# Optimization experiments

Hardware: AMD Instinct MI355X
Metric: run time of the kernel (lower is better)

The kernel has to match this reference:

```python
import jax, jax.numpy as jnp
import numpy as np

B, S, D, H = 2, 2048, 1024, 16
DK = D // H


def setup_inputs() -> dict:
    key = jax.random.key(0)
    ks = jax.random.split(key, 14)
    inp = {
        'query': jax.random.normal(ks[0], (B, S, D), jnp.float32),
        'key': jax.random.normal(ks[1], (B, S, D), jnp.float32),
        'value': jax.random.normal(ks[2], (B, S, D), jnp.float32),
        'mask': jax.random.randint(ks[3], (B, 1, S, S), 0, 2).astype(bool),
        'rel_pos_bias': jax.random.normal(ks[4], (1, H, S, S), jnp.float32),
    }
    scale = 1.0 / np.sqrt(D)
    names = ['Wq', 'bq', 'Wk', 'bk', 'Wv', 'bv', 'Wo', 'bo']
    for i, n in enumerate(names):
        k = ks[5 + i]
        if n.startswith('W'):
            inp[n] = jax.random.normal(k, (D, D), jnp.float32) * scale
        else:
            inp[n] = jnp.zeros((D,), jnp.float32)
    return inp


def reference(query, key, value, mask, rel_pos_bias, Wq, bq, Wk, bk, Wv, bv, Wo, bo):
    # torch Linear: y = x @ W^T + b; W stored [out, in]
    def proj(x, W, b):
        y = x @ W.T + b                       # [B,S,D]
        return y.reshape(B, S, H, DK).transpose(0, 2, 1, 3)  # [B,H,S,DK]

    q = proj(query, Wq, bq)
    k = proj(key, Wk, bk)
    v = proj(value, Wv, bv)

    scores = jnp.einsum('bhqd,bhkd->bhqk', q, k) / jnp.sqrt(jnp.float32(DK))
    scores = scores + rel_pos_bias
    scores = jnp.where(mask, jnp.float32(-1e9), scores)
    p_attn = jax.nn.softmax(scores, axis=-1)
    x = jnp.einsum('bhqk,bhkd->bhqd', p_attn, v)  # [B,H,S,DK]
    x = x.transpose(0, 2, 1, 3).reshape(B, S, D)
    return x @ Wo.T + bo
```

## Files before the change

### kernel.cpp

```cpp
#include <hip/hip_runtime.h>
#include <stdint.h>


typedef _Float16 f16;
typedef _Float16 f16x8 __attribute__((ext_vector_type(8)));
typedef _Float16 f16x4 __attribute__((ext_vector_type(4)));
typedef float f32x4 __attribute__((ext_vector_type(4)));

#define LOG2E 1.44269504088896340736f

__device__ __forceinline__ void gload16(const void* g, void* l) {
  __builtin_amdgcn_global_load_lds(
      (const __attribute__((address_space(1))) unsigned int*)g,
      (__attribute__((address_space(3))) unsigned int*)l, 16, 0, 0);
}

struct CvtSrcs { const float* s[7]; };

__global__ __launch_bounds__(256) void cvt_all(CvtSrcs a, f16* __restrict__ out) {
  const int i = blockIdx.x * 256 + threadIdx.x;
  int r, base;
  if (i < 3145728) { r = i >> 20; base = r << 20; }
  else { r = 3 + ((i - 3145728) >> 18); base = 3145728 + ((r - 3) << 18); }
  const float4 v = ((const float4*)a.s[r])[i - base];
  f16x4 o = {(f16)v.x, (f16)v.y, (f16)v.z, (f16)v.w};
  ((f16x4*)out)[i] = o;
}

__global__ void mask_detect(const uint8_t* __restrict__ m, int* __restrict__ flag) {
  __shared__ int s_off, s_weird;
  const int t = threadIdx.x;
  if (t == 0) { s_off = 0; s_weird = 0; }
  __syncthreads();
  int f_off = 0, f_weird = 0;
  for (int i = t; i < 8192; i += 256) {
    const uint8_t v = m[i];
    if ((i & 3) && v) f_off = 1;
    if (v > 1) f_weird = 1;
  }
  if (f_off) atomicOr(&s_off, 1);
  if (f_weird) atomicOr(&s_weird, 1);
  __syncthreads();
  if (t == 0) *flag = (s_off && !s_weird) ? 1 : 0;
}

__global__ __launch_bounds__(256) void mask_canon(const uint8_t* __restrict__ m,
                                                  uint8_t* __restrict__ out,
                                                  const int* __restrict__ flag) {
  const int i = (blockIdx.x * 256 + threadIdx.x) * 4;
  uchar4 o;
  if (*flag) {
    const uchar4 v = *(const uchar4*)(m + i);
    o = make_uchar4(v.x != 0, v.y != 0, v.z != 0, v.w != 0);
  } else {
    const int4 v = *(const int4*)((const int*)m + i);
    o = make_uchar4(v.x != 0, v.y != 0, v.z != 0, v.w != 0);
  }
  *(uchar4*)(out + i) = o;
}

__global__ __launch_bounds__(256, 2) void gemm_qkv(
    const f16* __restrict__ qh, const f16* __restrict__ kh, const f16* __restrict__ vh,
    const f16* __restrict__ wq, const f16* __restrict__ wk, const f16* __restrict__ wv,
    const float* __restrict__ bq, const float* __restrict__ bk, const float* __restrict__ bv,
    f16* __restrict__ Qp, f16* __restrict__ Kp, f16* __restrict__ Vt) {
  constexpr int K = 1024;
  const int t = threadIdx.x;
  const int w = t >> 6, lane = t & 63, l15 = lane & 15, l4 = lane >> 4;
  const int nt = (int)blockIdx.x % 48;
  const int bm = ((int)blockIdx.x / 48) * 128;
  const int which = nt >> 4;
  const int bn = (nt & 15) * 64;
  const f16* A = which == 0 ? qh : which == 1 ? kh : vh;
  const f16* Bw = which == 0 ? wq : which == 1 ? wk : wv;
  const float* bias = which == 0 ? bq : which == 1 ? bk : bv;

  __shared__ f16 As[2][128 * 32];
  __shared__ f16 Bs[2][64 * 32];

  const f16* a0 = A + (size_t)(bm + (t >> 2)) * K + (t & 3) * 8;
  const f16* a1 = a0 + (size_t)64 * K;
  const f16* b0 = Bw + (size_t)(bn + (t >> 2)) * K + (t & 3) * 8;

  f32x4 acc[2][4];
#pragma unroll
  for (int m = 0; m < 2; ++m)
#pragma unroll
    for (int n = 0; n < 4; ++n) acc[m][n] = (f32x4){0.f, 0.f, 0.f, 0.f};

#define STAGE_G(buf, k0)                          \
  do {                                            \
    gload16(a0 + (k0), &As[buf][w * 512]);        \
    gload16(a1 + (k0), &As[buf][2048 + w * 512]); \
    gload16(b0 + (k0), &Bs[buf][w * 512]);        \
  } while (0)

  STAGE_G(0, 0);
  __syncthreads();
  int cur = 0;
#pragma unroll 1
  for (int kt = 0; kt < 32; ++kt) {
    if (kt < 31) STAGE_G(cur ^ 1, (kt + 1) * 32);
    const f16* ap = &As[cur][(w * 32 + l15) * 32 + l4 * 8];
    const f16* bp = &Bs[cur][l15 * 32 + l4 * 8];
    f16x8 af[2], bfr[4];
#pragma unroll
    for (int m = 0; m < 2; ++m) af[m] = *(const f16x8*)(ap + m * 512);
#pragma unroll
    for (int n = 0; n < 4; ++n) bfr[n] = *(const f16x8*)(bp + n * 512);
#pragma unroll
    for (int m = 0; m < 2; ++m)
#pragma unroll
      for (int n = 0; n < 4; ++n)
        acc[m][n] = __builtin_amdgcn_mfma_f32_16x16x32_f16(af[m], bfr[n], acc[m][n], 0, 0, 0);
    __syncthreads();
    cur ^= 1;
  }
#undef STAGE_G

  const float scale = which == 0 ? 0.125f * LOG2E : 1.0f;
  f16* outp = which == 0 ? Qp : which == 1 ? Kp : Vt;
#pragma unroll
  for (int m = 0; m < 2; ++m) {
    const int r0 = bm + w * 32 + m * 16 + (l4 << 2);
#pragma unroll
    for (int n = 0; n < 4; ++n) {
      const int c = bn + n * 16 + l15;
      const float bv = bias[c];
#pragma unroll
      for (int j = 0; j < 4; ++j) {
        const int r = r0 + j;
        const float v = (acc[m][n][j] + bv) * scale;
        const int b_ = r >> 11, s = r & 2047, h_ = c >> 6, dk = c & 63;
        if (which < 2)
          outp[(((size_t)b_ * 16 + h_) * 2048 + s) * 64 + dk] = (f16)v;
        else
          outp[(((size_t)b_ * 16 + h_) * 64 + dk) * 2048 + s] = (f16)v;
      }
    }
  }
}

__global__ __launch_bounds__(256, 2) void gemm_out(const f16* __restrict__ A,
                                                   const f16* __restrict__ Bw,
                                                   const float* __restrict__ bias,
                                                   float* __restrict__ outp) {
  constexpr int K = 1024;
  const int t = threadIdx.x;
  const int w = t >> 6, lane = t & 63, l15 = lane & 15, l4 = lane >> 4;
  const int bm = (int)(blockIdx.x >> 4) * 128;
  const int bn = (int)(blockIdx.x & 15) * 64;

  __shared__ f16 As[2][128 * 32];
  __shared__ f16 Bs[2][64 * 32];

  const f16* a0 = A + (size_t)(bm + (t >> 2)) * K + (t & 3) * 8;
  const f16* a1 = a0 + (size_t)64 * K;
  const f16* b0 = Bw + (size_t)(bn + (t >> 2)) * K + (t & 3) * 8;

  f32x4 acc[2][4];
#pragma unroll
  for (int m = 0; m < 2; ++m)
#pragma unroll
    for (int n = 0; n < 4; ++n) acc[m][n] = (f32x4){0.f, 0.f, 0.f, 0.f};

#define STAGE_G(buf, k0)                          \
  do {                                            \
    gload16(a0 + (k0), &As[buf][w * 512]);        \
    gload16(a1 + (k0), &As[buf][2048 + w * 512]); \
    gload16(b0 + (k0), &Bs[buf][w * 512]);        \
  } while (0)

  STAGE_G(0, 0);
  __syncthreads();
  int cur = 0;
#pragma unroll 1
  for (int kt = 0; kt < 32; ++kt) {
    if (kt < 31) STAGE_G(cur ^ 1, (kt + 1) * 32);
    const f16* ap = &As[cur][(w * 32 + l15) * 32 + l4 * 8];
    const f16* bp = &Bs[cur][l15 * 32 + l4 * 8];
    f16x8 af[2], bfr[4];
#pragma unroll
    for (int m = 0; m < 2; ++m) af[m] = *(const f16x8*)(ap + m * 512);
#pragma unroll
    for (int n = 0; n < 4; ++n) bfr[n] = *(const f16x8*)(bp + n * 512);
#pragma unroll
    for (int m = 0; m < 2; ++m)
#pragma unroll
      for (int n = 0; n < 4; ++n)
        acc[m][n] = __builtin_amdgcn_mfma_f32_16x16x32_f16(af[m], bfr[n], acc[m][n], 0, 0, 0);
    __syncthreads();
    cur ^= 1;
  }
#undef STAGE_G

#pragma unroll
  for (int m = 0; m < 2; ++m) {
    const int r0 = bm + w * 32 + m * 16 + (l4 << 2);
#pragma unroll
    for (int n = 0; n < 4; ++n) {
      const int c = bn + n * 16 + l15;
      const float bv = bias[c];
#pragma unroll
      for (int j = 0; j < 4; ++j)
        outp[(size_t)(r0 + j) * 1024 + c] = acc[m][n][j] + bv;
    }
  }
}

__device__ __forceinline__ const f16x8* swzr(const f16* base, int row, int bytecol) {
  return (const f16x8*)((const char*)base + row * 128 + (bytecol ^ ((row & 7) << 4)));
}

__global__ __launch_bounds__(256, 4) void attn_fwd(
    const f16* __restrict__ Qp, const f16* __restrict__ Kp,
    const f16* __restrict__ Vt, const float* __restrict__ bias,
    const uint8_t* __restrict__ mask, f16* __restrict__ X) {
  constexpr int S = 2048;
  const int bid = blockIdx.x;
  const int qt = bid & 31, b = (bid >> 5) & 1, h = bid >> 6;
  const int t = threadIdx.x, w = t >> 6, lane = t & 63;
  const int l15 = lane & 15, l4 = lane >> 4;
  const int q0 = qt * 64 + w * 16;

  const f16* Qbh = Qp + (size_t)(b * 16 + h) * S * 64;
  const f16* Kbh = Kp + (size_t)(b * 16 + h) * S * 64;
  const f16* Vbh = Vt + (size_t)(b * 16 + h) * 64 * S;
  const float* biasr = bias + (size_t)h * S * S + (size_t)(q0 + l15) * S + l4 * 4;
  const uint8_t* maskr = mask + (size_t)b * S * S + (size_t)(q0 + l15) * S + l4 * 4;

  __shared__ f16 Ks[2][64 * 64];
  __shared__ f16 Vs[2][64 * 64];
  __shared__ f16 Ps[4][16 * 64];

  f16x8 qf[2];
#pragma unroll
  for (int ks = 0; ks < 2; ++ks)
    qf[ks] = *(const f16x8*)(Qbh + (size_t)(q0 + l15) * 64 + ks * 32 + l4 * 8);

  f32x4 oacc[4];
#pragma unroll
  for (int n = 0; n < 4; ++n) oacc[n] = (f32x4){0.f, 0.f, 0.f, 0.f};
  float mrow = -3e38f, lrow = 0.f;

  const int srow = t >> 3;
  const int scol = (((t & 7) ^ (srow & 7)) << 3);

#define STAGE(bf, kk)                                                               \
  do {                                                                              \
    gload16(Kbh + (size_t)((kk) + srow) * 64 + scol, &Ks[bf][w * 512]);             \
    gload16(Kbh + (size_t)((kk) + 32 + srow) * 64 + scol, &Ks[bf][2048 + w * 512]); \
    gload16(Vbh + (size_t)srow * S + (kk) + scol, &Vs[bf][w * 512]);                \
    gload16(Vbh + (size_t)(32 + srow) * S + (kk) + scol, &Vs[bf][2048 + w * 512]);  \
  } while (0)

  STAGE(0, 0);
  STAGE(1, 64);

#pragma unroll 1
  for (int kt = 0; kt < 32; ++kt) {
    const int k0 = kt * 64;
    const int buf = kt & 1;
    asm volatile("s_waitcnt vmcnt(4)" ::: "memory");
    __builtin_amdgcn_s_barrier();

    f32x4 bc[4];
    uint32_t mc[4];
#pragma unroll
    for (int n = 0; n < 4; ++n) {
      bc[n] = *(const f32x4*)(biasr + k0 + n * 16);
      mc[n] = *(const uint32_t*)(maskr + k0 + n * 16);
    }

    f32x4 sacc[4];
#pragma unroll
    for (int n = 0; n < 4; ++n) sacc[n] = (f32x4){0.f, 0.f, 0.f, 0.f};
#pragma unroll
    for (int n = 0; n < 4; ++n)
#pragma unroll
      for (int ks = 0; ks < 2; ++ks) {
        const f16x8 kf = *swzr(&Ks[buf][0], n * 16 + l15, ks * 64 + l4 * 16);
        sacc[n] = __builtin_amdgcn_mfma_f32_16x16x32_f16(kf, qf[ks], sacc[n], 0, 0, 0);
      }

    float tmax = -3e38f;
#pragma unroll
    for (int n = 0; n < 4; ++n)
#pragma unroll
      for (int j = 0; j < 4; ++j) {
        float s = fmaf(bc[n][j], LOG2E, sacc[n][j]);
        s = ((mc[n] >> (8 * j)) & 255u) ? -1.44269504e9f : s;
        sacc[n][j] = s;
        tmax = fmaxf(tmax, s);
      }
    tmax = fmaxf(tmax, __shfl_xor(tmax, 16));
    tmax = fmaxf(tmax, __shfl_xor(tmax, 32));

    const float mnew = fmaxf(mrow, tmax);
    const float alpha = __builtin_exp2f(mrow - mnew);
    mrow = mnew;
    float lsum = 0.f;
#pragma unroll
    for (int n = 0; n < 4; ++n)
#pragma unroll
      for (int j = 0; j < 4; ++j) {
        const float e = __builtin_exp2f(sacc[n][j] - mnew);
        sacc[n][j] = e;
        lsum += e;
      }
    lsum += __shfl_xor(lsum, 16);
    lsum += __shfl_xor(lsum, 32);
    lrow = lrow * alpha + lsum;

    float aq[4];
#pragma unroll
    for (int j = 0; j < 4; ++j) aq[j] = __shfl(alpha, l4 * 4 + j);
#pragma unroll
    for (int n = 0; n < 4; ++n)
#pragma unroll
      for (int j = 0; j < 4; ++j) oacc[n][j] *= aq[j];

#pragma unroll
    for (int n = 0; n < 4; ++n) {
      f16x4 pk = {(f16)sacc[n][0], (f16)sacc[n][1], (f16)sacc[n][2], (f16)sacc[n][3]};
      *(f16x4*)((char*)&Ps[w][0] + l15 * 128 +
                ((32 * n + 8 * l4) ^ ((l15 & 7) << 4))) = pk;
    }

    f16x8 pf[2];
#pragma unroll
    for (int ks = 0; ks < 2; ++ks) pf[ks] = *swzr(&Ps[w][0], l15, ks * 64 + l4 * 16);
#pragma unroll
    for (int ks = 0; ks < 2; ++ks)
#pragma unroll
      for (int n = 0; n < 4; ++n) {
        const f16x8 vf = *swzr(&Vs[buf][0], n * 16 + l15, ks * 64 + l4 * 16);
        oacc[n] = __builtin_amdgcn_mfma_f32_16x16x32_f16(pf[ks], vf, oacc[n], 0, 0, 0);
      }

    __builtin_amdgcn_s_barrier();
    STAGE(buf, (k0 + 128) & (S - 1));
  }
#undef STAGE

  asm volatile("s_waitcnt vmcnt(0)" ::: "memory");

  const float inv = 1.0f / lrow;
  float invq[4];
#pragma unroll
  for (int j = 0; j < 4; ++j) invq[j] = __shfl(inv, l4 * 4 + j);
#pragma unroll
  for (int j = 0; j < 4; ++j) {
    const int qrow = q0 + l4 * 4 + j;
#pragma unroll
    for (int n = 0; n < 4; ++n)
      X[((size_t)b * 2048 + qrow) * 1024 + h * 64 + n * 16 + l15] =
          (f16)(oacc[n][j] * invq[j]);
  }
}

extern "C" void kernel_launch(void* const* d_in, const int* in_sizes, int n_in,
                              void* d_out, int out_size, void* d_ws, size_t ws_size,
                              hipStream_t stream) {
  const float* query = (const float*)d_in[0];
  const float* key_ = (const float*)d_in[1];
  const float* value = (const float*)d_in[2];
  const uint8_t* mask = (const uint8_t*)d_in[3];
  const float* bias = (const float*)d_in[4];
  const float* Wq = (const float*)d_in[5];
  const float* bq = (const float*)d_in[6];
  const float* Wk = (const float*)d_in[7];
  const float* bk = (const float*)d_in[8];
  const float* Wv = (const float*)d_in[9];
  const float* bv = (const float*)d_in[10];
  const float* Wo = (const float*)d_in[11];
  const float* bo = (const float*)d_in[12];

  char* p = (char*)d_ws;
  f16* qh = (f16*)p; p += (size_t)4194304 * 2;
  f16* kh = (f16*)p; p += (size_t)4194304 * 2;
  f16* vh = (f16*)p; p += (size_t)4194304 * 2;
  f16* wqh = (f16*)p; p += (size_t)1048576 * 2;
  f16* wkh = (f16*)p; p += (size_t)1048576 * 2;
  f16* wvh = (f16*)p; p += (size_t)1048576 * 2;
  f16* woh = (f16*)p; p += (size_t)1048576 * 2;
  f16* Qp = (f16*)p; p += (size_t)4194304 * 2;
  f16* Kp = (f16*)p; p += (size_t)4194304 * 2;
  f16* Vt = (f16*)p; p += (size_t)4194304 * 2;
  f16* Xh = (f16*)p; p += (size_t)4194304 * 2;
  uint8_t* m8 = (uint8_t*)p; p += (size_t)8388608;
  int* flag = (int*)p; p += 256;
  if (ws_size < (size_t)(p - (char*)d_ws)) return;

  mask_detect<<<1, 256, 0, stream>>>(mask, flag);
  mask_canon<<<8192, 256, 0, stream>>>(mask, m8, flag);

  CvtSrcs cs;
  cs.s[0] = query; cs.s[1] = key_; cs.s[2] = value;
  cs.s[3] = Wq; cs.s[4] = Wk; cs.s[5] = Wv; cs.s[6] = Wo;
  cvt_all<<<16384, 256, 0, stream>>>(cs, qh);

  gemm_qkv<<<1536, 256, 0, stream>>>(qh, kh, vh, wqh, wkh, wvh, bq, bk, bv,
                                     Qp, Kp, Vt);

  attn_fwd<<<1024, 256, 0, stream>>>(Qp, Kp, Vt, bias, m8, Xh);

  gemm_out<<<512, 256, 0, stream>>>(Xh, woh, bo, (float*)d_out);
}
```

Before: 288.5 us.

## Share rel-pos bias across batches in attention, add lazy rescale and packed conversion

The attention kernel now runs 512 threads per block, covering both batch items for the same head and query tile, so that the two batch halves read the same rel_pos_bias rows in close succession and can share them through cache. K/V staging is now single-buffered per batch, with a __syncthreads on each side, which removes the double-buffer prefetch overlap. Softmax gains a lazy max-update that skips rescaling when the new max stays within a threshold, branchless masking via fmaf, and packed RTZ f16 conversion. The GEMM launch bounds are raised to three blocks per SM. The risks are less load/compute overlap, register pressure from the higher occupancy target, and slightly different rounding.

After: 291.1 us. About the same (+0.9%).

```diff
diff --git a/kernel.cpp b/kernel.cpp
--- a/kernel.cpp
+++ b/kernel.cpp
@@ -5,6 +5,7 @@
 typedef _Float16 f16;
 typedef _Float16 f16x8 __attribute__((ext_vector_type(8)));
 typedef _Float16 f16x4 __attribute__((ext_vector_type(4)));
+typedef __fp16 h2 __attribute__((ext_vector_type(2)));
 typedef float f32x4 __attribute__((ext_vector_type(4)));
 
 #define LOG2E 1.44269504088896340736f
@@ -59,7 +60,7 @@
   *(uchar4*)(out + i) = o;
 }
 
-__global__ __launch_bounds__(256, 2) void gemm_qkv(
+__global__ __launch_bounds__(256, 3) void gemm_qkv(
     const f16* __restrict__ qh, const f16* __restrict__ kh, const f16* __restrict__ vh,
     const f16* __restrict__ wq, const f16* __restrict__ wk, const f16* __restrict__ wv,
     const float* __restrict__ bq, const float* __restrict__ bk, const float* __restrict__ bv,
@@ -141,7 +142,7 @@
   }
 }
 
-__global__ __launch_bounds__(256, 2) void gemm_out(const f16* __restrict__ A,
+__global__ __launch_bounds__(256, 3) void gemm_out(const f16* __restrict__ A,
                                                    const f16* __restrict__ Bw,
                                                    const float* __restrict__ bias,
                                                    float* __restrict__ outp) {
@@ -212,26 +213,29 @@
   return (const f16x8*)((const char*)base + row * 128 + (bytecol ^ ((row & 7) << 4)));
 }
 
-__global__ __launch_bounds__(256, 4) void attn_fwd(
+__global__ __launch_bounds__(512, 4) void attn_fwd(
     const f16* __restrict__ Qp, const f16* __restrict__ Kp,
     const f16* __restrict__ Vt, const float* __restrict__ bias,
     const uint8_t* __restrict__ mask, f16* __restrict__ X) {
   constexpr int S = 2048;
   const int bid = blockIdx.x;
-  const int qt = bid & 31, b = (bid >> 5) & 1, h = bid >> 6;
+  const int qt = bid & 31, h = bid >> 5;
   const int t = threadIdx.x, w = t >> 6, lane = t & 63;
   const int l15 = lane & 15, l4 = lane >> 4;
-  const int q0 = qt * 64 + w * 16;
-
-  const f16* Qbh = Qp + (size_t)(b * 16 + h) * S * 64;
-  const f16* Kbh = Kp + (size_t)(b * 16 + h) * S * 64;
-  const f16* Vbh = Vt + (size_t)(b * 16 + h) * 64 * S;
+  const int bb = w >> 2;
+  const int q0 = qt * 64 + (w & 3) * 16;
+
+  const f16* Qbh = Qp + (size_t)(bb * 16 + h) * S * 64;
+  const f16* Kb0 = Kp + (size_t)h * S * 64;
+  const f16* Kb1 = Kp + (size_t)(16 + h) * S * 64;
+  const f16* Vb0 = Vt + (size_t)h * 64 * S;
+  const f16* Vb1 = Vt + (size_t)(16 + h) * 64 * S;
   const float* biasr = bias + (size_t)h * S * S + (size_t)(q0 + l15) * S + l4 * 4;
-  const uint8_t* maskr = mask + (size_t)b * S * S + (size_t)(q0 + l15) * S + l4 * 4;
+  const uint8_t* mr = mask + (size_t)bb * S * S + (size_t)(q0 + l15) * S + l4 * 4;
 
   __shared__ f16 Ks[2][64 * 64];
   __shared__ f16 Vs[2][64 * 64];
-  __shared__ f16 Ps[4][16 * 64];
+  __shared__ f16 Ps[8][16 * 64];
 
   f16x8 qf[2];
 #pragma unroll
@@ -246,31 +250,27 @@
   const int srow = t >> 3;
   const int scol = (((t & 7) ^ (srow & 7)) << 3);
 
-#define STAGE(bf, kk)                                                               \
-  do {                                                                              \
-    gload16(Kbh + (size_t)((kk) + srow) * 64 + scol, &Ks[bf][w * 512]);             \
-    gload16(Kbh + (size_t)((kk) + 32 + srow) * 64 + scol, &Ks[bf][2048 + w * 512]); \
-    gload16(Vbh + (size_t)srow * S + (kk) + scol, &Vs[bf][w * 512]);                \
-    gload16(Vbh + (size_t)(32 + srow) * S + (kk) + scol, &Vs[bf][2048 + w * 512]);  \
+#define STAGE(kk)                                                       \
+  do {                                                                  \
+    gload16(Kb0 + (size_t)((kk) + srow) * 64 + scol, &Ks[0][w * 512]);  \
+    gload16(Kb1 + (size_t)((kk) + srow) * 64 + scol, &Ks[1][w * 512]);  \
+    gload16(Vb0 + (size_t)srow * S + (kk) + scol, &Vs[0][w * 512]);     \
+    gload16(Vb1 + (size_t)srow * S + (kk) + scol, &Vs[1][w * 512]);     \
   } while (0)
 
-  STAGE(0, 0);
-  STAGE(1, 64);
+  STAGE(0);
 
 #pragma unroll 1
   for (int kt = 0; kt < 32; ++kt) {
     const int k0 = kt * 64;
-    const int buf = kt & 1;
-    asm volatile("s_waitcnt vmcnt(4)" ::: "memory");
-    __builtin_amdgcn_s_barrier();
-
     f32x4 bc[4];
     uint32_t mc[4];
 #pragma unroll
     for (int n = 0; n < 4; ++n) {
       bc[n] = *(const f32x4*)(biasr + k0 + n * 16);
-      mc[n] = *(const uint32_t*)(maskr + k0 + n * 16);
-    }
+      mc[n] = *(const uint32_t*)(mr + k0 + n * 16);
+    }
+    __syncthreads();
 
     f32x4 sacc[4];
 #pragma unroll
@@ -279,71 +279,78 @@
     for (int n = 0; n < 4; ++n)
 #pragma unroll
       for (int ks = 0; ks < 2; ++ks) {
-        const f16x8 kf = *swzr(&Ks[buf][0], n * 16 + l15, ks * 64 + l4 * 16);
+        const f16x8 kf = *swzr(&Ks[bb][0], n * 16 + l15, ks * 64 + l4 * 16);
         sacc[n] = __builtin_amdgcn_mfma_f32_16x16x32_f16(kf, qf[ks], sacc[n], 0, 0, 0);
       }
 
-    float tmax = -3e38f;
-#pragma unroll
-    for (int n = 0; n < 4; ++n)
+    float tm[4];
+#pragma unroll
+    for (int n = 0; n < 4; ++n) {
 #pragma unroll
       for (int j = 0; j < 4; ++j) {
-        float s = fmaf(bc[n][j], LOG2E, sacc[n][j]);
-        s = ((mc[n] >> (8 * j)) & 255u) ? -1.44269504e9f : s;
-        sacc[n][j] = s;
-        tmax = fmaxf(tmax, s);
+        const float mf = (float)((mc[n] >> (8 * j)) & 255u);
+        sacc[n][j] = fmaf(mf, -2e9f, fmaf(bc[n][j], LOG2E, sacc[n][j]));
       }
+      tm[n] = fmaxf(fmaxf(sacc[n][0], sacc[n][1]), fmaxf(sacc[n][2], sacc[n][3]));
+    }
+    float tmax = fmaxf(fmaxf(tm[0], tm[1]), fmaxf(tm[2], tm[3]));
     tmax = fmaxf(tmax, __shfl_xor(tmax, 16));
     tmax = fmaxf(tmax, __shfl_xor(tmax, 32));
 
-    const float mnew = fmaxf(mrow, tmax);
-    const float alpha = __builtin_exp2f(mrow - mnew);
-    mrow = mnew;
-    float lsum = 0.f;
-#pragma unroll
-    for (int n = 0; n < 4; ++n)
-#pragma unroll
-      for (int j = 0; j < 4; ++j) {
-        const float e = __builtin_exp2f(sacc[n][j] - mnew);
-        sacc[n][j] = e;
-        lsum += e;
-      }
+    if (!__all(tmax <= mrow + 11.5f)) {
+      const float mnew = fmaxf(mrow, tmax);
+      const float alpha = __builtin_exp2f(mrow - mnew);
+      mrow = mnew;
+      lrow *= alpha;
+      float aq[4];
+#pragma unroll
+      for (int j = 0; j < 4; ++j) aq[j] = __shfl(alpha, l4 * 4 + j);
+#pragma unroll
+      for (int n = 0; n < 4; ++n)
+#pragma unroll
+        for (int j = 0; j < 4; ++j) oacc[n][j] *= aq[j];
+    }
+
+    float ls[4];
+#pragma unroll
+    for (int n = 0; n < 4; ++n) {
+#pragma unroll
+      for (int j = 0; j < 4; ++j)
+        sacc[n][j] = __builtin_exp2f(sacc[n][j] - mrow);
+      ls[n] = (sacc[n][0] + sacc[n][1]) + (sacc[n][2] + sacc[n][3]);
+    }
+    float lsum = (ls[0] + ls[1]) + (ls[2] + ls[3]);
     lsum += __shfl_xor(lsum, 16);
     lsum += __shfl_xor(lsum, 32);
-    lrow = lrow * alpha + lsum;
-
-    float aq[4];
-#pragma unroll
-    for (int j = 0; j < 4; ++j) aq[j] = __shfl(alpha, l4 * 4 + j);
-#pragma unroll
-    for (int n = 0; n < 4; ++n)
-#pragma unroll
-      for (int j = 0; j < 4; ++j) oacc[n][j] *= aq[j];
-
-#pragma unroll
-    for (int n = 0; n < 4; ++n) {
-      f16x4 pk = {(f16)sacc[n][0], (f16)sacc[n][1], (f16)sacc[n][2], (f16)sacc[n][3]};
-      *(f16x4*)((char*)&Ps[w][0] + l15 * 128 +
+    lrow += lsum;
+
+#pragma unroll
+    for (int n = 0; n < 4; ++n) {
+      const h2 p01 = __builtin_amdgcn_cvt_pkrtz(sacc[n][0], sacc[n][1]);
+      const h2 p23 = __builtin_amdgcn_cvt_pkrtz(sacc[n][2], sacc[n][3]);
+      uint2 pk;
+      pk.x = __builtin_bit_cast(unsigned int, p01);
+      pk.y = __builtin_bit_cast(unsigned int, p23);
+      *(uint2*)((char*)&Ps[w][0] + l15 * 128 +
                 ((32 * n + 8 * l4) ^ ((l15 & 7) << 4))) = pk;
     }
 
     f16x8 pf[2];
 #pragma unroll
-    for (int ks = 0; ks < 2; ++ks) pf[ks] = *swzr(&Ps[w][0], l15, ks * 64 + l4 * 16);
-#pragma unroll
     for (int ks = 0; ks < 2; ++ks)
+      pf[ks] = *swzr(&Ps[w][0], l15, ks * 64 + l4 * 16);
+#pragma unroll
+    for (int ks = 0; ks < 2; ++ks)
 #pragma unroll
       for (int n = 0; n < 4; ++n) {
-        const f16x8 vf = *swzr(&Vs[buf][0], n * 16 + l15, ks * 64 + l4 * 16);
+        const f16x8 vf = *swzr(&Vs[bb][0], n * 16 + l15, ks * 64 + l4 * 16);
         oacc[n] = __builtin_amdgcn_mfma_f32_16x16x32_f16(pf[ks], vf, oacc[n], 0, 0, 0);
       }
 
-    __builtin_amdgcn_s_barrier();
-    STAGE(buf, (k0 + 128) & (S - 1));
+    __syncthreads();
+    if (kt < 31) STAGE(k0 + 64);
   }
 #undef STAGE
-
-  asm volatile("s_waitcnt vmcnt(0)" ::: "memory");
 
   const float inv = 1.0f / lrow;
   float invq[4];
@@ -354,7 +361,7 @@
     const int qrow = q0 + l4 * 4 + j;
 #pragma unroll
     for (int n = 0; n < 4; ++n)
-      X[((size_t)b * 2048 + qrow) * 1024 + h * 64 + n * 16 + l15] =
+      X[((size_t)bb * 2048 + qrow) * 1024 + h * 64 + n * 16 + l15] =
           (f16)(oacc[n][j] * invq[j]);
   }
 }
@@ -403,7 +410,7 @@
   gemm_qkv<<<1536, 256, 0, stream>>>(qh, kh, vh, wqh, wkh, wvh, bq, bk, bv,
                                      Qp, Kp, Vt);
 
-  attn_fwd<<<1024, 256, 0, stream>>>(Qp, Kp, Vt, bias, m8, Xh);
+  attn_fwd<<<512, 512, 0, stream>>>(Qp, Kp, Vt, bias, m8, Xh);
 
   gemm_out<<<512, 256, 0, stream>>>(Xh, woh, bo, (float*)d_out);
 }
```
